# Kernel optimization log

Measured on AMD Instinct MI355X. Metric: run time of the kernel, lower is better.

The kernel has to match this reference:

```python
import jax, jax.numpy as jnp
import numpy as np

NEG = -1.0e4  # log-semiring additive identity (Semiring.zero)


def setup_inputs() -> dict:
    key = jax.random.key(0)
    k1, k2 = jax.random.split(key)
    B, L, T = 32, 512, 64
    logits = jax.random.normal(k1, (B, L, T), dtype=jnp.float32)
    mask = jnp.ones((B, L), dtype=bool)
    # xavier_normal init for [T, T]: std = sqrt(2 / (T + T)) = 1/sqrt(T)
    transitions = jax.random.normal(k2, (T, T), dtype=jnp.float32) * (1.0 / np.sqrt(T))
    return {"logits": logits, "mask": mask, "transitions": transitions}


def _crf_log_partition(logits, mask, transitions):
    B, L, T = logits.shape
    maskf = mask.astype(logits.dtype)
    logits = logits * maskf[..., None]                       # zero masked positions
    m = maskf[:, 1:, None, None]                             # [B, L-1, 1, 1]
    trans = transitions[None, None] * m                      # [B, L-1, T, T]
    # potentials[b, t, i, j] = logits[b, t+1, j] + transitions[i, j]
    potentials = logits[:, 1:, None, :] + trans
    # masked steps are replaced by the log-semiring identity matrix
    eye = jnp.where(jnp.eye(T, dtype=bool), 0.0, NEG).astype(logits.dtype)
    potentials = potentials * m + eye * (1.0 - m)            # [B, L-1, T, T]

    start = logits[:, 0]                                     # [B, T]

    def step(alpha, P):
        # alpha: [B, T] (log-space), P: [B, T, T]
        # alpha'[j] = logsumexp_i alpha[i] + P[i, j]
        return jax.nn.logsumexp(alpha[:, :, None] + P, axis=1), None

    Pseq = jnp.moveaxis(potentials, 1, 0)                    # [L-1, B, T, T]
    alpha, _ = jax.lax.scan(step, start, Pseq)
    return jax.nn.logsumexp(alpha, axis=-1)                  # [B]


def reference(logits, mask, transitions):
    return _crf_log_partition(logits, mask, transitions)
```

## Files before the change

### kernel.cpp

```cpp
#include <hip/hip_runtime.h>
#include <hip/hip_bf16.h>


#define LL 512
#define TT 64
#define CHUNKS 16
#define SS (LL / CHUNKS)

typedef __attribute__((ext_vector_type(4))) short short4v;
typedef __attribute__((ext_vector_type(4))) float float4v;

__device__ __forceinline__ float4v mfma16(short4v a, short4v b, float4v c) {
#if defined(__HIP_DEVICE_COMPILE__)
    return __builtin_amdgcn_mfma_f32_16x16x16bf16_1k(a, b, c, 0, 0, 0);
#else
    return c;
#endif
}

__device__ __forceinline__ float rdlane_f(float v, int lane) {
    return __int_as_float(__builtin_amdgcn_readlane(__float_as_int(v), lane));
}
__device__ __forceinline__ float bf2f(unsigned short u) {
    return __uint_as_float(((unsigned int)u) << 16);
}
__device__ __forceinline__ short f2bf(float f) {
    __hip_bfloat16 h = __float2bfloat16(f);
    return *reinterpret_cast<short*>(&h);
}

__global__ __launch_bounds__(64, 1) void crf_chunk(
    const float* __restrict__ logits,
    const float* __restrict__ trans,
    unsigned short* __restrict__ Mws,
    float* __restrict__ lsws)
{
    __shared__ float sh_g[TT];
    const int L = threadIdx.x;
    const int c = L & 15;
    const int q = L >> 4;
    const int bid = blockIdx.x;
    const int w  = bid & 3;
    const int cc = (bid >> 2) & (CHUNKS - 1);
    const int b  = bid >> 6;

    short4v Af[4][4];
#pragma unroll
    for (int jt = 0; jt < 4; ++jt) {
#pragma unroll
        for (int kt = 0; kt < 4; ++kt) {
            short4v v;
#pragma unroll
            for (int e = 0; e < 4; ++e) {
                const int k = kt * 16 + 4 * q + e;
                const int m = jt * 16 + c;
                v[e] = f2bf(__expf(trans[k * TT + m]));
            }
            Af[jt][kt] = v;
        }
    }

    const int rg = w * 16 + c;
    short4v Nf[4];
#pragma unroll
    for (int kt = 0; kt < 4; ++kt) {
        short4v v;
#pragma unroll
        for (int e = 0; e < 4; ++e)
            v[e] = f2bf((kt * 16 + 4 * q + e == rg) ? 1.0f : 0.0f);
        Nf[kt] = v;
    }

    float ls = 0.0f;
    const float* lgb = logits + (size_t)b * (LL * TT);
    const int tb = (cc == 0) ? 1 : cc * SS;
    const int te = cc * SS + SS;

    for (int t = tb; t < te; ++t) {
        sh_g[L] = __expf(lgb[t * TT + L]);
        __syncthreads();

        float4v y[4];
#pragma unroll
        for (int jt = 0; jt < 4; ++jt) {
            float4v a = {0.f, 0.f, 0.f, 0.f};
            a = mfma16(Af[jt][0], Nf[0], a);
            a = mfma16(Af[jt][1], Nf[1], a);
            a = mfma16(Af[jt][2], Nf[2], a);
            a = mfma16(Af[jt][3], Nf[3], a);
            y[jt] = a;
        }

        float mx = 0.0f;
#pragma unroll
        for (int jt = 0; jt < 4; ++jt) {
            const float4v g4 = *reinterpret_cast<const float4v*>(&sh_g[jt * 16 + 4 * q]);
            y[jt] = y[jt] * g4;
            mx = fmaxf(mx, fmaxf(fmaxf(y[jt][0], y[jt][1]), fmaxf(y[jt][2], y[jt][3])));
        }
        mx = fmaxf(mx, __shfl_xor(mx, 16));
        mx = fmaxf(mx, __shfl_xor(mx, 32));
        const float sc = __builtin_amdgcn_rcpf(mx);
        ls += __logf(mx);

#pragma unroll
        for (int jt = 0; jt < 4; ++jt) {
            short4v v;
            v[0] = f2bf(y[jt][0] * sc);
            v[1] = f2bf(y[jt][1] * sc);
            v[2] = f2bf(y[jt][2] * sc);
            v[3] = f2bf(y[jt][3] * sc);
            Nf[jt] = v;
        }
        __syncthreads();
    }

    unsigned short* mp = Mws + ((size_t)(b * CHUNKS + cc) * TT + rg) * TT;
#pragma unroll
    for (int kt = 0; kt < 4; ++kt)
        *reinterpret_cast<short4v*>(mp + kt * 16 + 4 * q) = Nf[kt];
    if (q == 0) lsws[(b * CHUNKS + cc) * TT + rg] = ls;
}

__global__ __launch_bounds__(64, 1) void crf_combine(
    const float* __restrict__ logits,
    const unsigned short* __restrict__ Mws,
    const float* __restrict__ lsws,
    float* __restrict__ out)
{
    const int b = blockIdx.x;
    const int j = threadIdx.x;

    float A = logits[(size_t)b * (LL * TT) + j];

    for (int cc = 0; cc < CHUNKS; ++cc) {
        const float tv = A + lsws[(b * CHUNKS + cc) * TT + j];
        float K = tv;
#pragma unroll
        for (int off = 32; off; off >>= 1) K = fmaxf(K, __shfl_xor(K, off));
        const float wv = __expf(tv - K);

        const unsigned short* Mp = Mws + (size_t)(b * CHUNKS + cc) * (TT * TT) + j;
        float s0 = 0.f, s1 = 0.f, s2 = 0.f, s3 = 0.f;
#pragma unroll
        for (int r = 0; r < TT; r += 4) {
            s0 = fmaf(rdlane_f(wv, r + 0), bf2f(Mp[(r + 0) * TT]), s0);
            s1 = fmaf(rdlane_f(wv, r + 1), bf2f(Mp[(r + 1) * TT]), s1);
            s2 = fmaf(rdlane_f(wv, r + 2), bf2f(Mp[(r + 2) * TT]), s2);
            s3 = fmaf(rdlane_f(wv, r + 3), bf2f(Mp[(r + 3) * TT]), s3);
        }
        A = K + __logf((s0 + s1) + (s2 + s3));
    }

    float K = A;
#pragma unroll
    for (int off = 32; off; off >>= 1) K = fmaxf(K, __shfl_xor(K, off));
    float e = __expf(A - K);
#pragma unroll
    for (int off = 32; off; off >>= 1) e += __shfl_xor(e, off);
    if (j == 0) out[b] = K + __logf(e);
}

extern "C" void kernel_launch(void* const* d_in, const int* in_sizes, int n_in,
                              void* d_out, int out_size, void* d_ws, size_t ws_size,
                              hipStream_t stream) {
    const float* logits = (const float*)d_in[0];
    const float* trans  = (const float*)d_in[2];
    float* out = (float*)d_out;

    const int B = in_sizes[1] / LL;

    unsigned short* Mws = (unsigned short*)d_ws;
    float* lsws = (float*)((char*)d_ws + (size_t)B * CHUNKS * TT * TT * sizeof(unsigned short));

    crf_chunk<<<dim3(B * CHUNKS * 4), dim3(64), 0, stream>>>(logits, trans, Mws, lsws);
    crf_combine<<<dim3(B), dim3(64), 0, stream>>>(logits, Mws, lsws, out);
}
```

Before: 97.53 us.

## Prefetch logits, amortize renormalization, transpose chunk matrices and double-buffer combine loads

```diff
diff --git a/kernel.cpp b/kernel.cpp
--- a/kernel.cpp
+++ b/kernel.cpp
@@ -8,6 +8,7 @@
 #define SS (LL / CHUNKS)
 
 typedef __attribute__((ext_vector_type(4))) short short4v;
+typedef __attribute__((ext_vector_type(8))) short short8v;
 typedef __attribute__((ext_vector_type(4))) float float4v;
 
 __device__ __forceinline__ float4v mfma16(short4v a, short4v b, float4v c) {
@@ -24,9 +25,12 @@
 __device__ __forceinline__ float bf2f(unsigned short u) {
     return __uint_as_float(((unsigned int)u) << 16);
 }
-__device__ __forceinline__ short f2bf(float f) {
+__device__ __forceinline__ short f2bf_rne(float f) {
     __hip_bfloat16 h = __float2bfloat16(f);
     return *reinterpret_cast<short*>(&h);
+}
+__device__ __forceinline__ short f2bf_t(float f) {
+    return (short)(__float_as_uint(f) >> 16);
 }
 
 __global__ __launch_bounds__(64, 1) void crf_chunk(
@@ -54,7 +58,7 @@
             for (int e = 0; e < 4; ++e) {
                 const int k = kt * 16 + 4 * q + e;
                 const int m = jt * 16 + c;
-                v[e] = f2bf(__expf(trans[k * TT + m]));
+                v[e] = f2bf_rne(__expf(trans[k * TT + m]));
             }
             Af[jt][kt] = v;
         }
@@ -67,7 +71,7 @@
         short4v v;
 #pragma unroll
         for (int e = 0; e < 4; ++e)
-            v[e] = f2bf((kt * 16 + 4 * q + e == rg) ? 1.0f : 0.0f);
+            v[e] = f2bf_rne((kt * 16 + 4 * q + e == rg) ? 1.0f : 0.0f);
         Nf[kt] = v;
     }
 
@@ -76,9 +80,12 @@
     const int tb = (cc == 0) ? 1 : cc * SS;
     const int te = cc * SS + SS;
 
+    float gv = lgb[tb * TT + L];
+
     for (int t = tb; t < te; ++t) {
-        sh_g[L] = __expf(lgb[t * TT + L]);
-        __syncthreads();
+        sh_g[L] = __expf(gv);
+        const int tn = (t + 1 < LL) ? (t + 1) : t;
+        gv = lgb[tn * TT + L];
 
         float4v y[4];
 #pragma unroll
@@ -91,35 +98,80 @@
             y[jt] = a;
         }
 
-        float mx = 0.0f;
 #pragma unroll
         for (int jt = 0; jt < 4; ++jt) {
             const float4v g4 = *reinterpret_cast<const float4v*>(&sh_g[jt * 16 + 4 * q]);
             y[jt] = y[jt] * g4;
-            mx = fmaxf(mx, fmaxf(fmaxf(y[jt][0], y[jt][1]), fmaxf(y[jt][2], y[jt][3])));
-        }
-        mx = fmaxf(mx, __shfl_xor(mx, 16));
-        mx = fmaxf(mx, __shfl_xor(mx, 32));
-        const float sc = __builtin_amdgcn_rcpf(mx);
-        ls += __logf(mx);
-
-#pragma unroll
-        for (int jt = 0; jt < 4; ++jt) {
-            short4v v;
-            v[0] = f2bf(y[jt][0] * sc);
-            v[1] = f2bf(y[jt][1] * sc);
-            v[2] = f2bf(y[jt][2] * sc);
-            v[3] = f2bf(y[jt][3] * sc);
-            Nf[jt] = v;
-        }
-        __syncthreads();
-    }
-
-    unsigned short* mp = Mws + ((size_t)(b * CHUNKS + cc) * TT + rg) * TT;
+        }
+
+        if ((t & 3) == 3) {
+            float mx = 0.0f;
+#pragma unroll
+            for (int jt = 0; jt < 4; ++jt)
+                mx = fmaxf(mx, fmaxf(fmaxf(y[jt][0], y[jt][1]), fmaxf(y[jt][2], y[jt][3])));
+            mx = fmaxf(mx, __shfl_xor(mx, 16));
+            mx = fmaxf(mx, __shfl_xor(mx, 32));
+            const float sc = __builtin_amdgcn_rcpf(mx);
+            ls += __logf(mx);
+#pragma unroll
+            for (int jt = 0; jt < 4; ++jt) {
+                short4v v;
+                v[0] = f2bf_t(y[jt][0] * sc);
+                v[1] = f2bf_t(y[jt][1] * sc);
+                v[2] = f2bf_t(y[jt][2] * sc);
+                v[3] = f2bf_t(y[jt][3] * sc);
+                Nf[jt] = v;
+            }
+        } else {
+#pragma unroll
+            for (int jt = 0; jt < 4; ++jt) {
+                short4v v;
+                v[0] = f2bf_t(y[jt][0]);
+                v[1] = f2bf_t(y[jt][1]);
+                v[2] = f2bf_t(y[jt][2]);
+                v[3] = f2bf_t(y[jt][3]);
+                Nf[jt] = v;
+            }
+        }
+    }
+
+    unsigned short* mp = Mws + (size_t)(b * CHUNKS + cc) * (TT * TT);
 #pragma unroll
     for (int kt = 0; kt < 4; ++kt)
-        *reinterpret_cast<short4v*>(mp + kt * 16 + 4 * q) = Nf[kt];
+#pragma unroll
+        for (int e = 0; e < 4; ++e)
+            mp[(kt * 16 + 4 * q + e) * TT + rg] = (unsigned short)Nf[kt][e];
     if (q == 0) lsws[(b * CHUNKS + cc) * TT + rg] = ls;
+}
+
+__device__ __forceinline__ void loadch(const unsigned short* __restrict__ Mws,
+                                       const float* __restrict__ lsws,
+                                       int idx, int j, short8v (&buf)[8], float& lsv) {
+    const short8v* row = reinterpret_cast<const short8v*>(Mws + ((size_t)idx * TT + j) * TT);
+#pragma unroll
+    for (int rb = 0; rb < 8; ++rb) buf[rb] = row[rb];
+    lsv = lsws[idx * TT + j];
+}
+
+__device__ __forceinline__ float foldch(float A, float lsv, const short8v (&buf)[8]) {
+    const float tv = A + lsv;
+    float K = tv;
+#pragma unroll
+    for (int off = 32; off; off >>= 1) K = fmaxf(K, __shfl_xor(K, off));
+    const float wv = __expf(tv - K);
+    float s0 = 0.f, s1 = 0.f, s2 = 0.f, s3 = 0.f;
+#pragma unroll
+    for (int rb = 0; rb < 8; ++rb) {
+        s0 = fmaf(rdlane_f(wv, rb * 8 + 0), bf2f((unsigned short)buf[rb][0]), s0);
+        s1 = fmaf(rdlane_f(wv, rb * 8 + 1), bf2f((unsigned short)buf[rb][1]), s1);
+        s2 = fmaf(rdlane_f(wv, rb * 8 + 2), bf2f((unsigned short)buf[rb][2]), s2);
+        s3 = fmaf(rdlane_f(wv, rb * 8 + 3), bf2f((unsigned short)buf[rb][3]), s3);
+        s0 = fmaf(rdlane_f(wv, rb * 8 + 4), bf2f((unsigned short)buf[rb][4]), s0);
+        s1 = fmaf(rdlane_f(wv, rb * 8 + 5), bf2f((unsigned short)buf[rb][5]), s1);
+        s2 = fmaf(rdlane_f(wv, rb * 8 + 6), bf2f((unsigned short)buf[rb][6]), s2);
+        s3 = fmaf(rdlane_f(wv, rb * 8 + 7), bf2f((unsigned short)buf[rb][7]), s3);
+    }
+    return K + __logf((s0 + s1) + (s2 + s3));
 }
 
 __global__ __launch_bounds__(64, 1) void crf_combine(
@@ -130,26 +182,20 @@
 {
     const int b = blockIdx.x;
     const int j = threadIdx.x;
+    const int bch = b * CHUNKS;
+
+    short8v bA[8], bB[8];
+    float lsA, lsB;
+    loadch(Mws, lsws, bch + 0, j, bA, lsA);
 
     float A = logits[(size_t)b * (LL * TT) + j];
 
-    for (int cc = 0; cc < CHUNKS; ++cc) {
-        const float tv = A + lsws[(b * CHUNKS + cc) * TT + j];
-        float K = tv;
-#pragma unroll
-        for (int off = 32; off; off >>= 1) K = fmaxf(K, __shfl_xor(K, off));
-        const float wv = __expf(tv - K);
-
-        const unsigned short* Mp = Mws + (size_t)(b * CHUNKS + cc) * (TT * TT) + j;
-        float s0 = 0.f, s1 = 0.f, s2 = 0.f, s3 = 0.f;
-#pragma unroll
-        for (int r = 0; r < TT; r += 4) {
-            s0 = fmaf(rdlane_f(wv, r + 0), bf2f(Mp[(r + 0) * TT]), s0);
-            s1 = fmaf(rdlane_f(wv, r + 1), bf2f(Mp[(r + 1) * TT]), s1);
-            s2 = fmaf(rdlane_f(wv, r + 2), bf2f(Mp[(r + 2) * TT]), s2);
-            s3 = fmaf(rdlane_f(wv, r + 3), bf2f(Mp[(r + 3) * TT]), s3);
-        }
-        A = K + __logf((s0 + s1) + (s2 + s3));
+#pragma unroll
+    for (int p = 0; p < CHUNKS / 2; ++p) {
+        loadch(Mws, lsws, bch + 2 * p + 1, j, bB, lsB);
+        A = foldch(A, lsA, bA);
+        if (2 * p + 2 < CHUNKS) loadch(Mws, lsws, bch + 2 * p + 2, j, bA, lsA);
+        A = foldch(A, lsB, bB);
     }
 
     float K = A;
```

After: 90.35 us. -7.4%, faster.

## Halve chunks, prefetch logits, renormalize every four steps, double-buffer combine loads

Applied to the files above, without the earlier changes.

```diff
diff --git a/kernel.cpp b/kernel.cpp
--- a/kernel.cpp
+++ b/kernel.cpp
@@ -4,7 +4,7 @@
 
 #define LL 512
 #define TT 64
-#define CHUNKS 16
+#define CHUNKS 8
 #define SS (LL / CHUNKS)
 
 typedef __attribute__((ext_vector_type(4))) short short4v;
@@ -17,7 +17,6 @@
     return c;
 #endif
 }
-
 __device__ __forceinline__ float rdlane_f(float v, int lane) {
     return __int_as_float(__builtin_amdgcn_readlane(__float_as_int(v), lane));
 }
@@ -35,14 +34,14 @@
     unsigned short* __restrict__ Mws,
     float* __restrict__ lsws)
 {
-    __shared__ float sh_g[TT];
+    __shared__ float sh_g[2][TT];
     const int L = threadIdx.x;
     const int c = L & 15;
     const int q = L >> 4;
     const int bid = blockIdx.x;
     const int w  = bid & 3;
     const int cc = (bid >> 2) & (CHUNKS - 1);
-    const int b  = bid >> 6;
+    const int b  = bid >> 5;
 
     short4v Af[4][4];
 #pragma unroll
@@ -76,9 +75,21 @@
     const int tb = (cc == 0) ? 1 : cc * SS;
     const int te = cc * SS + SS;
 
+    float n1 = lgb[(tb + 1) * TT + L];
+    float n2 = lgb[(tb + 2) * TT + L];
+    float n3 = lgb[(tb + 3) * TT + L];
+    sh_g[tb & 1][L] = __expf(lgb[tb * TT + L]);
+
     for (int t = tb; t < te; ++t) {
-        sh_g[L] = __expf(lgb[t * TT + L]);
-        __syncthreads();
+        float4v gx[4];
+#pragma unroll
+        for (int jt = 0; jt < 4; ++jt)
+            gx[jt] = *reinterpret_cast<const float4v*>(&sh_g[t & 1][jt * 16 + 4 * q]);
+
+        sh_g[(t + 1) & 1][L] = __expf(n1);
+        n1 = n2; n2 = n3;
+        const int tn = (t + 4 < LL) ? (t + 4) : (LL - 1);
+        n3 = lgb[tn * TT + L];
 
         float4v y[4];
 #pragma unroll
@@ -91,35 +102,73 @@
             y[jt] = a;
         }
 
-        float mx = 0.0f;
-#pragma unroll
-        for (int jt = 0; jt < 4; ++jt) {
-            const float4v g4 = *reinterpret_cast<const float4v*>(&sh_g[jt * 16 + 4 * q]);
-            y[jt] = y[jt] * g4;
-            mx = fmaxf(mx, fmaxf(fmaxf(y[jt][0], y[jt][1]), fmaxf(y[jt][2], y[jt][3])));
+#pragma unroll
+        for (int jt = 0; jt < 4; ++jt) y[jt] = y[jt] * gx[jt];
+
+        if ((t & 3) == 3) {
+            float mx = 0.0f;
+#pragma unroll
+            for (int jt = 0; jt < 4; ++jt)
+                mx = fmaxf(mx, fmaxf(fmaxf(y[jt][0], y[jt][1]), fmaxf(y[jt][2], y[jt][3])));
+            mx = fmaxf(mx, __shfl_xor(mx, 16));
+            mx = fmaxf(mx, __shfl_xor(mx, 32));
+            const float sc = __builtin_amdgcn_rcpf(mx);
+            ls += __logf(mx);
+#pragma unroll
+            for (int jt = 0; jt < 4; ++jt) {
+                short4v v;
+                v[0] = f2bf(y[jt][0] * sc);
+                v[1] = f2bf(y[jt][1] * sc);
+                v[2] = f2bf(y[jt][2] * sc);
+                v[3] = f2bf(y[jt][3] * sc);
+                Nf[jt] = v;
+            }
+        } else {
+#pragma unroll
+            for (int jt = 0; jt < 4; ++jt) {
+                short4v v;
+                v[0] = f2bf(y[jt][0]);
+                v[1] = f2bf(y[jt][1]);
+                v[2] = f2bf(y[jt][2]);
+                v[3] = f2bf(y[jt][3]);
+                Nf[jt] = v;
+            }
         }
-        mx = fmaxf(mx, __shfl_xor(mx, 16));
-        mx = fmaxf(mx, __shfl_xor(mx, 32));
-        const float sc = __builtin_amdgcn_rcpf(mx);
-        ls += __logf(mx);
-
-#pragma unroll
-        for (int jt = 0; jt < 4; ++jt) {
-            short4v v;
-            v[0] = f2bf(y[jt][0] * sc);
-            v[1] = f2bf(y[jt][1] * sc);
-            v[2] = f2bf(y[jt][2] * sc);
-            v[3] = f2bf(y[jt][3] * sc);
-            Nf[jt] = v;
-        }
-        __syncthreads();
-    }
-
-    unsigned short* mp = Mws + ((size_t)(b * CHUNKS + cc) * TT + rg) * TT;
+    }
+
+    unsigned short* mp = Mws + (size_t)(b * CHUNKS + cc) * (TT * TT);
 #pragma unroll
     for (int kt = 0; kt < 4; ++kt)
-        *reinterpret_cast<short4v*>(mp + kt * 16 + 4 * q) = Nf[kt];
+#pragma unroll
+        for (int e = 0; e < 4; ++e)
+            mp[(kt * 16 + 4 * q + e) * TT + rg] = (unsigned short)Nf[kt][e];
     if (q == 0) lsws[(b * CHUNKS + cc) * TT + rg] = ls;
+}
+
+__device__ __forceinline__ void loadrow(const unsigned short* __restrict__ Mws,
+                                        const float* __restrict__ lsws,
+                                        int idx, int j, float (&m)[TT], float& lsv) {
+    const unsigned short* base = Mws + (size_t)idx * (TT * TT) + j;
+#pragma unroll
+    for (int i = 0; i < TT; ++i) m[i] = bf2f(base[i * TT]);
+    lsv = lsws[idx * TT + j];
+}
+
+__device__ __forceinline__ float foldrow(float A, float lsv, const float (&m)[TT]) {
+    const float tv = A + lsv;
+    float K = tv;
+#pragma unroll
+    for (int off = 32; off; off >>= 1) K = fmaxf(K, __shfl_xor(K, off));
+    const float wv = __expf(tv - K);
+    float s0 = 0.f, s1 = 0.f, s2 = 0.f, s3 = 0.f;
+#pragma unroll
+    for (int i = 0; i < TT; i += 4) {
+        s0 = fmaf(rdlane_f(wv, i + 0), m[i + 0], s0);
+        s1 = fmaf(rdlane_f(wv, i + 1), m[i + 1], s1);
+        s2 = fmaf(rdlane_f(wv, i + 2), m[i + 2], s2);
+        s3 = fmaf(rdlane_f(wv, i + 3), m[i + 3], s3);
+    }
+    return K + __logf((s0 + s1) + (s2 + s3));
 }
 
 __global__ __launch_bounds__(64, 1) void crf_combine(
@@ -130,26 +179,20 @@
 {
     const int b = blockIdx.x;
     const int j = threadIdx.x;
+    const int bch = b * CHUNKS;
+
+    float mA[TT], mB[TT];
+    float lsA, lsB;
+    loadrow(Mws, lsws, bch + 0, j, mA, lsA);
 
     float A = logits[(size_t)b * (LL * TT) + j];
 
-    for (int cc = 0; cc < CHUNKS; ++cc) {
-        const float tv = A + lsws[(b * CHUNKS + cc) * TT + j];
-        float K = tv;
-#pragma unroll
-        for (int off = 32; off; off >>= 1) K = fmaxf(K, __shfl_xor(K, off));
-        const float wv = __expf(tv - K);
-
-        const unsigned short* Mp = Mws + (size_t)(b * CHUNKS + cc) * (TT * TT) + j;
-        float s0 = 0.f, s1 = 0.f, s2 = 0.f, s3 = 0.f;
-#pragma unroll
-        for (int r = 0; r < TT; r += 4) {
-            s0 = fmaf(rdlane_f(wv, r + 0), bf2f(Mp[(r + 0) * TT]), s0);
-            s1 = fmaf(rdlane_f(wv, r + 1), bf2f(Mp[(r + 1) * TT]), s1);
-            s2 = fmaf(rdlane_f(wv, r + 2), bf2f(Mp[(r + 2) * TT]), s2);
-            s3 = fmaf(rdlane_f(wv, r + 3), bf2f(Mp[(r + 3) * TT]), s3);
-        }
-        A = K + __logf((s0 + s1) + (s2 + s3));
+#pragma unroll
+    for (int p = 0; p < CHUNKS / 2; ++p) {
+        loadrow(Mws, lsws, bch + 2 * p + 1, j, mB, lsB);
+        A = foldrow(A, lsA, mA);
+        if (2 * p + 2 < CHUNKS) loadrow(Mws, lsws, bch + 2 * p + 2, j, mA, lsA);
+        A = foldrow(A, lsB, mB);
     }
 
     float K = A;
```

Result: faster. 90.27 us (-7.4%).
